# Kernel tuning notes

Hardware: AMD Instinct MI355X
Metric: run time of the kernel (lower is better)

The kernel has to match this reference:

```python
import jax, jax.numpy as jnp
import numpy as np

B, N, EMB, NCLS = 4, 4096, 1024, 13

def knn_euclid(x, k):
    # x: (B,C,N); k nearest by squared euclidean distance
    sq = jnp.sum(x * x, axis=1)                        # (B,N)
    inner = jnp.einsum('bcn,bcm->bnm', x, x)           # (B,N,N)
    d = sq[:, :, None] - 2.0 * inner + sq[:, None, :]
    return jax.lax.stop_gradient(jax.lax.top_k(-d, k)[1])   # (B,N,k)

def knn_cosine(x, k):
    xn = x / (jnp.linalg.norm(x, axis=1, keepdims=True) + 1e-8)
    sim = jnp.einsum('bcn,bcm->bnm', xn, xn)           # (B,N,N)
    return jax.lax.stop_gradient(jax.lax.top_k(sim, k)[1])

def edge_conv(x, idx, w0, s0, o0, w1, s1, o1):
    # x: (B,C,N), idx: (B,N,k) -> (B,64,N). Edge feats = concat(x_j - x_i, x_i).
    xt = jnp.transpose(x, (0, 2, 1))                   # (B,N,C)
    nbr = jax.vmap(lambda f, i: f[i])(xt, idx)         # (B,N,k,C)
    ctr = jnp.broadcast_to(xt[:, :, None, :], nbr.shape)
    e = jnp.concatenate([nbr - ctr, ctr], axis=-1)     # (B,N,k,2C)
    h = jax.nn.leaky_relu(jnp.einsum('bnkc,oc->bnko', e, w0) * s0 + o0, 0.2)
    h = jax.nn.leaky_relu(jnp.einsum('bnkc,oc->bnko', h, w1) * s1 + o1, 0.2)
    return jnp.transpose(jnp.max(h, axis=2), (0, 2, 1))  # max over k -> (B,64,N)

def conv1d(x, w):
    return jnp.einsum('bcn,oc->bon', x, w)

def setup_inputs():
    key = jax.random.key(0)
    cnt = [0]
    def nxt():
        cnt[0] += 1
        return jax.random.fold_in(key, cnt[0])
    W = lambda shape: jax.random.normal(nxt(), shape, jnp.float32) * 0.05
    S = lambda n: 1.0 + 0.1 * jax.random.normal(nxt(), (n,), jnp.float32)   # folded BN scale
    O = lambda n: 0.05 * jax.random.normal(nxt(), (n,), jnp.float32)        # folded BN offset / bias
    inp = {'x': jax.random.normal(nxt(), (B, 6, N), jnp.float32)}
    inp.update(w1_0=W((64, 12)), s1_0=S(64), o1_0=O(64), w1_1=W((64, 64)), s1_1=S(64), o1_1=O(64))
    inp.update(w2_0=W((64, 128)), s2_0=S(64), o2_0=O(64), w2_1=W((64, 64)), s2_1=S(64), o2_1=O(64))
    inp.update(w3_0=W((64, 128)), s3_0=S(64), o3_0=O(64), w3_1=W((64, 64)), s3_1=S(64), o3_1=O(64))
    inp.update(w4=W((EMB, 192)), b4=O(EMB))
    inp.update(wf1=W((512, EMB + 192)), sf1=S(512), of1=O(512))
    inp.update(wf2=W((256, 512)), sf2=S(256), of2=O(256))
    inp.update(wf3=W((NCLS, 256)))
    inp['k'] = 20
    return inp

def reference(x, w1_0, s1_0, o1_0, w1_1, s1_1, o1_1,
              w2_0, s2_0, o2_0, w2_1, s2_1, o2_1,
              w3_0, s3_0, o3_0, w3_1, s3_1, o3_1,
              w4, b4, wf1, sf1, of1, wf2, sf2, of2, wf3, k):
    x1 = edge_conv(x, knn_euclid(x, k), w1_0, s1_0, o1_0, w1_1, s1_1, o1_1)
    x2 = edge_conv(x1, knn_cosine(x1, k), w2_0, s2_0, o2_0, w2_1, s2_1, o2_1)
    x3 = edge_conv(x2, knn_cosine(x2, k), w3_0, s3_0, o3_0, w3_1, s3_1, o3_1)
    xc = jnp.concatenate([x1, x2, x3], axis=1)         # (B,192,N)
    x4 = jax.nn.leaky_relu(conv1d(xc, w4) + b4[None, :, None], 0.2)  # (B,EMB,N)
    g = jnp.max(x4, axis=2, keepdims=True)             # global max pool (B,EMB,1)
    g = jnp.broadcast_to(g, (x4.shape[0], x4.shape[1], xc.shape[2]))  # Repeat to N
    x5 = jnp.concatenate([x1, x2, x3, g], axis=1)      # (B,192+EMB,N)
    h = jax.nn.leaky_relu(conv1d(x5, wf1) * sf1[None, :, None] + of1[None, :, None], 0.2)
    h = jax.nn.leaky_relu(conv1d(h, wf2) * sf2[None, :, None] + of2[None, :, None], 0.2)
    return conv1d(h, wf3)                              # (B,NCLS,N)
```

## Files before the change

### kernel.cpp

```cpp
#include <hip/hip_runtime.h>
#include <hip/hip_bf16.h>
#include <float.h>

#define NPTS 4096
#define NB 4
#define KNN 20

__device__ __forceinline__ float lrelu(float x) { return x > 0.f ? x : 0.2f * x; }

__device__ __forceinline__ void atomicMaxF(float* addr, float val) {
    int* ia = (int*)addr;
    int old = *ia;
    while (__int_as_float(old) < val) {
        int assumed = old;
        old = atomicCAS(ia, assumed, __float_as_int(val));
        if (old == assumed) break;
    }
}

__global__ void k_transp(const float* __restrict__ src, float* __restrict__ dst,
                         int rows, int srcld, int cols) {
    int i = blockIdx.x * 256 + threadIdx.x;
    if (i >= rows * cols) return;
    int r = i % rows, c = i / rows;
    dst[c * rows + r] = src[(size_t)r * srcld + c];
}

__global__ void k_sqnorm(const float* __restrict__ x, float* __restrict__ sq) {
    int i = blockIdx.x * 256 + threadIdx.x;
    int b = i >> 12, n = i & 4095;
    const float* xb = x + b * 6 * NPTS;
    float s = 0.f;
#pragma unroll
    for (int c = 0; c < 6; c++) { float v = xb[c * NPTS + n]; s += v * v; }
    sq[i] = s;
}

__global__ __launch_bounds__(256) void k_knn_euclid(const float* __restrict__ x,
                                                    const float* __restrict__ sq,
                                                    int* __restrict__ idx) {
    int t = threadIdx.x;
    int w = t >> 6, ln = t & 63;
    int qid = blockIdx.x * 4 + w;
    int b = qid >> 12, qn = qid & 4095;
    const float* xb = x + b * 6 * NPTS;
    const float* sqb = sq + b * NPTS;
    float q0 = xb[qn], q1 = xb[NPTS + qn], q2 = xb[2 * NPTS + qn];
    float q3 = xb[3 * NPTS + qn], q4 = xb[4 * NPTS + qn], q5 = xb[5 * NPTS + qn];
    float sqn = sqb[qn];
    float lv = -FLT_MAX; int li = 0x7fffffff;
    float th = -FLT_MAX;
    for (int t0 = 0; t0 < NPTS; t0 += 64) {
        int m = t0 + ln;
        float dot = q0 * xb[m] + q1 * xb[NPTS + m] + q2 * xb[2 * NPTS + m]
                  + q3 * xb[3 * NPTS + m] + q4 * xb[4 * NPTS + m] + q5 * xb[5 * NPTS + m];
        float sv = -(sqn - 2.f * dot + sqb[m]);
        unsigned long long mask = __ballot(sv > th);
        while (mask) {
            int src = __ffsll((unsigned long long)mask) - 1;
            mask &= mask - 1;
            float v = __shfl(sv, src);
            if (!(v > th)) continue;
            int mi = t0 + src;
            float pv = __shfl_up(lv, 1);
            int   pi = __shfl_up(li, 1);
            unsigned long long bm = __ballot(ln < 20 && lv >= v);
            int pos = __popcll(bm);
            if (ln < 20) {
                if (ln == pos) { lv = v; li = mi; }
                else if (ln > pos) { lv = pv; li = pi; }
            }
            th = __shfl(lv, 19);
        }
    }
    if (ln < KNN) idx[qid * KNN + ln] = li;
}

__global__ __launch_bounds__(256) void k_knn_cos(const float* __restrict__ xn,
                                                 const float* __restrict__ xnT,
                                                 int* __restrict__ idx) {
    __shared__ float xq[64][20];
    __shared__ float simb[16][520];
    int t = threadIdx.x;
    int w = t >> 6, ln = t & 63;
    int b = blockIdx.x >> 8;
    int q0blk = (blockIdx.x & 255) * 16;
    const float* xqg = xn + ((size_t)(b << 12) + q0blk) * 64;
    {
        int q = t >> 4, c4 = t & 15;
        float4 v = *(const float4*)(xqg + q * 64 + c4 * 4);
        xq[c4 * 4 + 0][q] = v.x; xq[c4 * 4 + 1][q] = v.y;
        xq[c4 * 4 + 2][q] = v.z; xq[c4 * 4 + 3][q] = v.w;
    }
    __syncthreads();
    int myq = w * 4;
    const float* xTb = xnT + (((size_t)b) << 12) * 64;
    float lv[4] = {-FLT_MAX, -FLT_MAX, -FLT_MAX, -FLT_MAX};
    int   li[4] = {0x7fffffff, 0x7fffffff, 0x7fffffff, 0x7fffffff};
    float th[4] = {-FLT_MAX, -FLT_MAX, -FLT_MAX, -FLT_MAX};
    for (int strip = 0; strip < 8; strip++) {
        int m0 = strip * 512 + ln * 8;
        float4 a0[4], a1[4];
#pragma unroll
        for (int q = 0; q < 4; q++) { a0[q] = (float4){0,0,0,0}; a1[q] = (float4){0,0,0,0}; }
        for (int c = 0; c < 64; c++) {
            const float* cr = xTb + (((size_t)c) << 12) + m0;
            float4 cv0 = *(const float4*)(cr);
            float4 cv1 = *(const float4*)(cr + 4);
            float4 qv = *(const float4*)&xq[c][myq];
            a0[0].x += qv.x * cv0.x; a0[0].y += qv.x * cv0.y; a0[0].z += qv.x * cv0.z; a0[0].w += qv.x * cv0.w;
            a1[0].x += qv.x * cv1.x; a1[0].y += qv.x * cv1.y; a1[0].z += qv.x * cv1.z; a1[0].w += qv.x * cv1.w;
            a0[1].x += qv.y * cv0.x; a0[1].y += qv.y * cv0.y; a0[1].z += qv.y * cv0.z; a0[1].w += qv.y * cv0.w;
            a1[1].x += qv.y * cv1.x; a1[1].y += qv.y * cv1.y; a1[1].z += qv.y * cv1.z; a1[1].w += qv.y * cv1.w;
            a0[2].x += qv.z * cv0.x; a0[2].y += qv.z * cv0.y; a0[2].z += qv.z * cv0.z; a0[2].w += qv.z * cv0.w;
            a1[2].x += qv.z * cv1.x; a1[2].y += qv.z * cv1.y; a1[2].z += qv.z * cv1.z; a1[2].w += qv.z * cv1.w;
            a0[3].x += qv.w * cv0.x; a0[3].y += qv.w * cv0.y; a0[3].z += qv.w * cv0.z; a0[3].w += qv.w * cv0.w;
            a1[3].x += qv.w * cv1.x; a1[3].y += qv.w * cv1.y; a1[3].z += qv.w * cv1.z; a1[3].w += qv.w * cv1.w;
        }
#pragma unroll
        for (int q = 0; q < 4; q++) {
            float mx8 = fmaxf(fmaxf(fmaxf(a0[q].x, a0[q].y), fmaxf(a0[q].z, a0[q].w)),
                              fmaxf(fmaxf(a1[q].x, a1[q].y), fmaxf(a1[q].z, a1[q].w)));
            unsigned long long gmask = __ballot(mx8 > th[q]);
            if (!gmask) continue;
            *(float4*)&simb[myq + q][ln * 8] = a0[q];
            *(float4*)&simb[myq + q][ln * 8 + 4] = a1[q];
            for (int j = 0; j < 8; j++) {
                if (!((gmask >> (8 * j)) & 0xffull)) continue;
                float sv = simb[myq + q][j * 64 + ln];
                int base = strip * 512 + j * 64;
                unsigned long long mask = __ballot(sv > th[q]);
                while (mask) {
                    int src = __ffsll((unsigned long long)mask) - 1;
                    mask &= mask - 1;
                    float v = __shfl(sv, src);
                    if (!(v > th[q])) continue;
                    int mi = base + src;
                    float pv = __shfl_up(lv[q], 1);
                    int   pi = __shfl_up(li[q], 1);
                    unsigned long long bm = __ballot(ln < 20 && lv[q] >= v);
                    int pos = __popcll(bm);
                    if (ln < 20) {
                        if (ln == pos) { lv[q] = v; li[q] = mi; }
                        else if (ln > pos) { lv[q] = pv; li[q] = pi; }
                    }
                    th[q] = __shfl(lv[q], 19);
                }
            }
        }
    }
#pragma unroll
    for (int q = 0; q < 4; q++) {
        if (ln < KNN) {
            int qid = (b << 12) + q0blk + myq + q;
            idx[(size_t)qid * KNN + ln] = li[q];
        }
    }
}

__global__ void k_normalize(const float* __restrict__ xcpm, int coff,
                            float* __restrict__ xn, float* __restrict__ xnT) {
    int pid = blockIdx.x * 256 + threadIdx.x;
    int b = pid >> 12, n = pid & 4095;
    const float* p = xcpm + (size_t)pid * 192 + coff;
    float s = 0.f;
#pragma unroll
    for (int c4 = 0; c4 < 16; c4++) {
        float4 v = *(const float4*)(p + c4 * 4);
        s += v.x * v.x + v.y * v.y + v.z * v.z + v.w * v.w;
    }
    float inv = 1.f / (sqrtf(s) + 1e-8f);
    float* q = xn + (size_t)pid * 64;
    float* qt = xnT + (((size_t)b) << 12) * 64 + n;
#pragma unroll
    for (int c4 = 0; c4 < 16; c4++) {
        float4 v = *(const float4*)(p + c4 * 4);
        float4 r; r.x = v.x * inv; r.y = v.y * inv; r.z = v.z * inv; r.w = v.w * inv;
        *(float4*)(q + c4 * 4) = r;
        qt[(size_t)(c4 * 4 + 0) << 12] = r.x;
        qt[(size_t)(c4 * 4 + 1) << 12] = r.y;
        qt[(size_t)(c4 * 4 + 2) << 12] = r.z;
        qt[(size_t)(c4 * 4 + 3) << 12] = r.w;
    }
}

__global__ __launch_bounds__(256) void k_edge1(const float* __restrict__ x,
    const float* __restrict__ w0, const float* __restrict__ s0, const float* __restrict__ o0,
    const float* __restrict__ w1, const float* __restrict__ s1, const float* __restrict__ o1,
    const int* __restrict__ idx, float* __restrict__ xcpm) {
    __shared__ float es[4][16];
    __shared__ float h0s[4][64];
    int t = threadIdx.x;
    int w = t >> 6, o = t & 63;
    int pid = blockIdx.x * 4 + w;
    int b = pid >> 12, n = pid & 4095;
    const float* xb = x + b * 6 * NPTS;
    float w0r[12];
    const float* w0p = w0 + o * 12;
#pragma unroll
    for (int c4 = 0; c4 < 3; c4++) {
        float4 v = *(const float4*)(w0p + c4 * 4);
        w0r[c4 * 4] = v.x; w0r[c4 * 4 + 1] = v.y; w0r[c4 * 4 + 2] = v.z; w0r[c4 * 4 + 3] = v.w;
    }
    float w1r[64];
    const float* w1p = w1 + o * 64;
#pragma unroll
    for (int c4 = 0; c4 < 16; c4++) {
        float4 v = *(const float4*)(w1p + c4 * 4);
        w1r[c4 * 4] = v.x; w1r[c4 * 4 + 1] = v.y; w1r[c4 * 4 + 2] = v.z; w1r[c4 * 4 + 3] = v.w;
    }
    float sv0 = s0[o], ov0 = o0[o], sv1 = s1[o], ov1 = o1[o];
    float cv = 0.f;
    if (o < 6) { cv = xb[o * NPTS + n]; es[w][6 + o] = cv; }
    if (o >= 12 && o < 16) es[w][o] = 0.f;
    float acc = -FLT_MAX;
    const int* ib = idx + pid * KNN;
    for (int kk = 0; kk < KNN; kk++) {
        int j = ib[kk] & 4095;
        if (o < 6) es[w][o] = xb[o * NPTS + j] - cv;
        float h = 0.f;
#pragma unroll
        for (int c4 = 0; c4 < 3; c4++) {
            float4 e4 = *(const float4*)&es[w][c4 * 4];
            h += w0r[c4 * 4] * e4.x + w0r[c4 * 4 + 1] * e4.y + w0r[c4 * 4 + 2] * e4.z + w0r[c4 * 4 + 3] * e4.w;
        }
        h = lrelu(h * sv0 + ov0);
        h0s[w][o] = h;
        float h2 = 0.f;
#pragma unroll
        for (int c4 = 0; c4 < 16; c4++) {
            float4 h4 = *(const float4*)&h0s[w][c4 * 4];
            h2 += w1r[c4 * 4] * h4.x + w1r[c4 * 4 + 1] * h4.y + w1r[c4 * 4 + 2] * h4.z + w1r[c4 * 4 + 3] * h4.w;
        }
        h2 = lrelu(h2 * sv1 + ov1);
        acc = fmaxf(acc, h2);
    }
    xcpm[(size_t)pid * 192 + o] = acc;
}

__global__ __launch_bounds__(256) void k_edge23(const float* __restrict__ xcpm,
    const float* __restrict__ w0, const float* __restrict__ s0, const float* __restrict__ o0,
    const float* __restrict__ w1, const float* __restrict__ s1, const float* __restrict__ o1,
    const int* __restrict__ idx, int ci, int co) {
    __shared__ float cs[4][64];
    __shared__ float es[4][64];
    __shared__ float h0s[4][64];
    int t = threadIdx.x;
    int w = t >> 6, o = t & 63;
    int pid = blockIdx.x * 4 + w;
    int b = pid >> 12;
    float w0r[64];
    const float* w0p = w0 + o * 128;
#pragma unroll
    for (int c4 = 0; c4 < 16; c4++) {
        float4 v = *(const float4*)(w0p + c4 * 4);
        w0r[c4 * 4] = v.x; w0r[c4 * 4 + 1] = v.y; w0r[c4 * 4 + 2] = v.z; w0r[c4 * 4 + 3] = v.w;
    }
    float w1r[64];
    const float* w1p = w1 + o * 64;
#pragma unroll
    for (int c4 = 0; c4 < 16; c4++) {
        float4 v = *(const float4*)(w1p + c4 * 4);
        w1r[c4 * 4] = v.x; w1r[c4 * 4 + 1] = v.y; w1r[c4 * 4 + 2] = v.z; w1r[c4 * 4 + 3] = v.w;
    }
    float sv0 = s0[o], ov0 = o0[o], sv1 = s1[o], ov1 = o1[o];
    float cv = xcpm[(size_t)pid * 192 + ci + o];
    cs[w][o] = cv;
    float h0b = 0.f;
    const float* w0q = w0p + 64;
#pragma unroll
    for (int c4 = 0; c4 < 16; c4++) {
        float4 wv = *(const float4*)(w0q + c4 * 4);
        float4 c4v = *(const float4*)&cs[w][c4 * 4];
        h0b += wv.x * c4v.x + wv.y * c4v.y + wv.z * c4v.z + wv.w * c4v.w;
    }
    float acc = -FLT_MAX;
    const int* ib = idx + pid * KNN;
    int j0 = ib[0] & 4095;
    float nv = xcpm[((size_t)(b * 4096 + j0)) * 192 + ci + o];
    for (int kk = 0; kk < KNN; kk++) {
        float cur = nv;
        if (kk < KNN - 1) {
            int jn = ib[kk + 1] & 4095;
            nv = xcpm[((size_t)(b * 4096 + jn)) * 192 + ci + o];
        }
        es[w][o] = cur - cv;
        float h = h0b;
#pragma unroll
        for (int c4 = 0; c4 < 16; c4++) {
            float4 e4 = *(const float4*)&es[w][c4 * 4];
            h += w0r[c4 * 4] * e4.x + w0r[c4 * 4 + 1] * e4.y + w0r[c4 * 4 + 2] * e4.z + w0r[c4 * 4 + 3] * e4.w;
        }
        h = lrelu(h * sv0 + ov0);
        h0s[w][o] = h;
        float h2 = 0.f;
#pragma unroll
        for (int c4 = 0; c4 < 16; c4++) {
            float4 h4 = *(const float4*)&h0s[w][c4 * 4];
            h2 += w1r[c4 * 4] * h4.x + w1r[c4 * 4 + 1] * h4.y + w1r[c4 * 4 + 2] * h4.z + w1r[c4 * 4 + 3] * h4.w;
        }
        h2 = lrelu(h2 * sv1 + ov1);
        acc = fmaxf(acc, h2);
    }
    float* outp = (float*)xcpm;
    outp[(size_t)pid * 192 + co + o] = acc;
}

__global__ void k_init_g(float* __restrict__ g) {
    g[blockIdx.x * 256 + threadIdx.x] = -FLT_MAX;
}

__global__ __launch_bounds__(256) void k_w4pool(const float* __restrict__ xc,
                                                const float* __restrict__ wT4,
                                                const float* __restrict__ b4,
                                                float* __restrict__ g) {
    __shared__ float xcs[192 * 68];
    int t = threadIdx.x;
    int b = blockIdx.y;
    int n0 = blockIdx.x * 64;
    const float* xb = xc + (size_t)(b * 4096 + n0) * 192;
    for (int i = t; i < 3072; i += 256) {
        int pt = i / 48, c4 = i - pt * 48;
        float4 v = *(const float4*)(xb + pt * 192 + c4 * 4);
        xcs[(c4 * 4 + 0) * 68 + pt] = v.x; xcs[(c4 * 4 + 1) * 68 + pt] = v.y;
        xcs[(c4 * 4 + 2) * 68 + pt] = v.z; xcs[(c4 * 4 + 3) * 68 + pt] = v.w;
    }
    __syncthreads();
    int o0 = (t >> 2) * 16, qd = t & 3;
    float4 bb[4];
#pragma unroll
    for (int k = 0; k < 4; k++) bb[k] = *(const float4*)(b4 + o0 + k * 4);
    float mx[16];
#pragma unroll
    for (int oo = 0; oo < 16; oo++) mx[oo] = -FLT_MAX;
    for (int sub = 0; sub < 4; sub++) {
        int tn0 = sub * 16 + qd * 4;
        float4 acc[16];
#pragma unroll
        for (int oo = 0; oo < 16; oo++) acc[oo] = (float4){0, 0, 0, 0};
        for (int c = 0; c < 192; c++) {
            float4 x4 = *(const float4*)&xcs[c * 68 + tn0];
            const float* wr = wT4 + c * 1024 + o0;
            float4 wq[4];
#pragma unroll
            for (int k = 0; k < 4; k++) wq[k] = *(const float4*)(wr + k * 4);
#pragma unroll
            for (int oo = 0; oo < 16; oo++) {
                float wv = ((const float*)wq)[oo];
                acc[oo].x += wv * x4.x; acc[oo].y += wv * x4.y;
                acc[oo].z += wv * x4.z; acc[oo].w += wv * x4.w;
            }
        }
#pragma unroll
        for (int oo = 0; oo < 16; oo++) {
            float bias = ((const float*)bb)[oo];
            float4 a = acc[oo];
            float h = fmaxf(fmaxf(lrelu(a.x + bias), lrelu(a.y + bias)),
                            fmaxf(lrelu(a.z + bias), lrelu(a.w + bias)));
            mx[oo] = fmaxf(mx[oo], h);
        }
    }
#pragma unroll
    for (int oo = 0; oo < 16; oo++) {
        float v = mx[oo];
        v = fmaxf(v, __shfl_xor(v, 1));
        v = fmaxf(v, __shfl_xor(v, 2));
        if (qd == 0) atomicMaxF(&g[b * 1024 + o0 + oo], v);
    }
}

__global__ __launch_bounds__(256) void k_goff(const float* __restrict__ g,
                                              const float* __restrict__ wf1,
                                              const float* __restrict__ sf1,
                                              const float* __restrict__ of1,
                                              float* __restrict__ goff) {
    int bo = blockIdx.x;
    int b = bo >> 9, o = bo & 511;
    int t = threadIdx.x;
    const float* wr = wf1 + (size_t)o * 1216 + 192;
    const float* gb = g + b * 1024;
    float s = 0.f;
    for (int c = t; c < 1024; c += 256) s += wr[c] * gb[c];
    __shared__ float red[4];
    for (int off = 32; off > 0; off >>= 1) s += __shfl_down(s, off);
    if ((t & 63) == 0) red[t >> 6] = s;
    __syncthreads();
    if (t == 0) {
        float tot = red[0] + red[1] + red[2] + red[3];
        goff[bo] = tot * sf1[o] + of1[o];
    }
}

#define TP 20
__global__ __launch_bounds__(256) void k_tail(const float* __restrict__ xc,
                                              const float* __restrict__ wf1T,
                                              const float* __restrict__ sf1,
                                              const float* __restrict__ goff,
                                              const float* __restrict__ wf2T,
                                              const float* __restrict__ sf2,
                                              const float* __restrict__ of2,
                                              const float* __restrict__ wf3,
                                              float* __restrict__ out) {
    __shared__ float xcs[192 * TP];
    __shared__ float h1s[512 * TP];
    __shared__ float h2s[256 * TP];
    int t = threadIdx.x;
    int b = blockIdx.y;
    int n0 = blockIdx.x * 16;
    const float* xb = xc + (size_t)(b * 4096 + n0) * 192;
    for (int i = t; i < 768; i += 256) {
        int pt = i / 48, c4 = i - pt * 48;
        float4 v = *(const float4*)(xb + pt * 192 + c4 * 4);
        xcs[(c4 * 4 + 0) * TP + pt] = v.x; xcs[(c4 * 4 + 1) * TP + pt] = v.y;
        xcs[(c4 * 4 + 2) * TP + pt] = v.z; xcs[(c4 * 4 + 3) * TP + pt] = v.w;
    }
    __syncthreads();
    {
        int o8 = (t >> 2) * 8, tn0 = (t & 3) * 4;
        float4 acc[8];
#pragma unroll
        for (int oo = 0; oo < 8; oo++) acc[oo] = (float4){0, 0, 0, 0};
        for (int c = 0; c < 192; c++) {
            float4 x4 = *(const float4*)&xcs[c * TP + tn0];
            const float* wr = wf1T + c * 512 + o8;
            float4 w0 = *(const float4*)(wr);
            float4 w1 = *(const float4*)(wr + 4);
            float wq[8] = {w0.x, w0.y, w0.z, w0.w, w1.x, w1.y, w1.z, w1.w};
#pragma unroll
            for (int oo = 0; oo < 8; oo++) {
                acc[oo].x += wq[oo] * x4.x; acc[oo].y += wq[oo] * x4.y;
                acc[oo].z += wq[oo] * x4.z; acc[oo].w += wq[oo] * x4.w;
            }
        }
#pragma unroll
        for (int oo = 0; oo < 8; oo++) {
            int o = o8 + oo;
            float s = sf1[o];
            float gv = goff[b * 512 + o];
            float4 r;
            r.x = lrelu(acc[oo].x * s + gv); r.y = lrelu(acc[oo].y * s + gv);
            r.z = lrelu(acc[oo].z * s + gv); r.w = lrelu(acc[oo].w * s + gv);
            *(float4*)&h1s[o * TP + tn0] = r;
        }
    }
    __syncthreads();
    {
        int o4 = (t >> 2) * 4, tn0 = (t & 3) * 4;
        float4 acc[4];
#pragma unroll
        for (int oo = 0; oo < 4; oo++) acc[oo] = (float4){0, 0, 0, 0};
        for (int c = 0; c < 512; c++) {
            float4 x4 = *(const float4*)&h1s[c * TP + tn0];
            float4 w = *(const float4*)(wf2T + c * 256 + o4);
            float wq[4] = {w.x, w.y, w.z, w.w};
#pragma unroll
            for (int oo = 0; oo < 4; oo++) {
                acc[oo].x += wq[oo] * x4.x; acc[oo].y += wq[oo] * x4.y;
                acc[oo].z += wq[oo] * x4.z; acc[oo].w += wq[oo] * x4.w;
            }
        }
#pragma unroll
        for (int oo = 0; oo < 4; oo++) {
            int o = o4 + oo;
            float s = sf2[o], of = of2[o];
            float4 r;
            r.x = lrelu(acc[oo].x * s + of); r.y = lrelu(acc[oo].y * s + of);
            r.z = lrelu(acc[oo].z * s + of); r.w = lrelu(acc[oo].w * s + of);
            *(float4*)&h2s[o * TP + tn0] = r;
        }
    }
    __syncthreads();
    if (t < 13 * 16) {
        int o = t >> 4, tn = t & 15;
        const float* wr = wf3 + o * 256;
        float acc = 0.f;
        for (int c4 = 0; c4 < 64; c4++) {
            float4 wv = *(const float4*)(wr + c4 * 4);
            acc += wv.x * h2s[(c4 * 4 + 0) * TP + tn] + wv.y * h2s[(c4 * 4 + 1) * TP + tn]
                 + wv.z * h2s[(c4 * 4 + 2) * TP + tn] + wv.w * h2s[(c4 * 4 + 3) * TP + tn];
        }
        out[((size_t)b * 13 + o) * NPTS + n0 + tn] = acc;
    }
}

extern "C" void kernel_launch(void* const* d_in, const int* in_sizes, int n_in,
                              void* d_out, int out_size, void* d_ws, size_t ws_size,
                              hipStream_t stream) {
    const float* x    = (const float*)d_in[0];
    const float* w1_0 = (const float*)d_in[1];
    const float* s1_0 = (const float*)d_in[2];
    const float* o1_0 = (const float*)d_in[3];
    const float* w1_1 = (const float*)d_in[4];
    const float* s1_1 = (const float*)d_in[5];
    const float* o1_1 = (const float*)d_in[6];
    const float* w2_0 = (const float*)d_in[7];
    const float* s2_0 = (const float*)d_in[8];
    const float* o2_0 = (const float*)d_in[9];
    const float* w2_1 = (const float*)d_in[10];
    const float* s2_1 = (const float*)d_in[11];
    const float* o2_1 = (const float*)d_in[12];
    const float* w3_0 = (const float*)d_in[13];
    const float* s3_0 = (const float*)d_in[14];
    const float* o3_0 = (const float*)d_in[15];
    const float* w3_1 = (const float*)d_in[16];
    const float* s3_1 = (const float*)d_in[17];
    const float* o3_1 = (const float*)d_in[18];
    const float* w4   = (const float*)d_in[19];
    const float* b4   = (const float*)d_in[20];
    const float* wf1  = (const float*)d_in[21];
    const float* sf1  = (const float*)d_in[22];
    const float* of1  = (const float*)d_in[23];
    const float* wf2  = (const float*)d_in[24];
    const float* sf2  = (const float*)d_in[25];
    const float* of2  = (const float*)d_in[26];
    const float* wf3  = (const float*)d_in[27];

    float* xcpm = (float*)d_ws;
    float* xn   = xcpm + (size_t)NB * NPTS * 192;
    float* sq   = xn + (size_t)NB * NPTS * 64;
    float* g    = sq + NB * NPTS;
    float* goff = g + NB * 1024;
    int*   idx  = (int*)(goff + NB * 512);
    float* wT4  = (float*)(idx + NB * NPTS * KNN);
    float* wf1T = wT4 + 192 * 1024;
    float* wf2T = wf1T + 192 * 512;
    float* xnT  = wf2T + 512 * 256;
    (void)in_sizes; (void)n_in; (void)out_size; (void)ws_size;

    k_transp<<<(1024 * 192 + 255) / 256, 256, 0, stream>>>(w4, wT4, 1024, 192, 192);
    k_transp<<<(512 * 192 + 255) / 256, 256, 0, stream>>>(wf1, wf1T, 512, 1216, 192);
    k_transp<<<(256 * 512 + 255) / 256, 256, 0, stream>>>(wf2, wf2T, 256, 512, 512);
    k_sqnorm<<<NB * NPTS / 256, 256, 0, stream>>>(x, sq);
    k_knn_euclid<<<NB * NPTS / 4, 256, 0, stream>>>(x, sq, idx);
    k_edge1<<<NB * NPTS / 4, 256, 0, stream>>>(x, w1_0, s1_0, o1_0, w1_1, s1_1, o1_1, idx, xcpm);
    k_normalize<<<NB * NPTS / 256, 256, 0, stream>>>(xcpm, 0, xn, xnT);
    k_knn_cos<<<NB * NPTS / 16, 256, 0, stream>>>(xn, xnT, idx);
    k_edge23<<<NB * NPTS / 4, 256, 0, stream>>>(xcpm, w2_0, s2_0, o2_0, w2_1, s2_1, o2_1, idx, 0, 64);
    k_normalize<<<NB * NPTS / 256, 256, 0, stream>>>(xcpm, 64, xn, xnT);
    k_knn_cos<<<NB * NPTS / 16, 256, 0, stream>>>(xn, xnT, idx);
    k_edge23<<<NB * NPTS / 4, 256, 0, stream>>>(xcpm, w3_0, s3_0, o3_0, w3_1, s3_1, o3_1, idx, 64, 128);
    k_init_g<<<NB * 1024 / 256, 256, 0, stream>>>(g);
    k_w4pool<<<dim3(NPTS / 64, NB), 256, 0, stream>>>(xcpm, wT4, b4, g);
    k_goff<<<NB * 512, 256, 0, stream>>>(g, wf1, sf1, of1, goff);
    k_tail<<<dim3(NPTS / 16, NB), 256, 0, stream>>>(xcpm, wf1T, sf1, goff, wf2T, sf2, of2, wf3, (float*)d_out);
}
```

Before: 1.532 ms.

## Compute cosine kNN similarity with split-bf16 MFMA instead of FP32 FMA

The cosine kNN similarity GEMM moves from scalar FP32 FMAs to bf16 MFMA 16x16x32 instructions. Normalized features are split into three bf16 parts (hi/mid/lo), and six cross products are accumulated to approximate FP32 accuracy. The normalize kernel now writes this packed bf16 layout instead of the fp32 and transposed copies. In exchange, the per-strip ballot early-skip is removed and two block barriers are added per strip. Small rounding differences could also change top-k tie ordering.

```diff
diff --git a/kernel.cpp b/kernel.cpp
--- a/kernel.cpp
+++ b/kernel.cpp
@@ -5,6 +5,11 @@
 #define NPTS 4096
 #define NB 4
 #define KNN 20
+
+typedef __attribute__((ext_vector_type(8))) short short8v;
+typedef __attribute__((ext_vector_type(4))) float f32x4;
+
+#define MFMA_B16(acc, a, b) acc = __builtin_amdgcn_mfma_f32_16x16x32_bf16((a), (b), (acc), 0, 0, 0)
 
 __device__ __forceinline__ float lrelu(float x) { return x > 0.f ? x : 0.2f * x; }
 
@@ -16,6 +21,11 @@
         old = atomicCAS(ia, assumed, __float_as_int(val));
         if (old == assumed) break;
     }
+}
+
+__device__ __forceinline__ unsigned bf16rne(float x) {
+    unsigned u = __float_as_uint(x);
+    return (u + 0x7fffu + ((u >> 16) & 1u)) >> 16;
 }
 
 __global__ void k_transp(const float* __restrict__ src, float* __restrict__ dst,
@@ -76,57 +86,73 @@
     if (ln < KNN) idx[qid * KNN + ln] = li;
 }
 
-__global__ __launch_bounds__(256) void k_knn_cos(const float* __restrict__ xn,
-                                                 const float* __restrict__ xnT,
+__global__ __launch_bounds__(256) void k_knn_cos(const unsigned short* __restrict__ xs,
                                                  int* __restrict__ idx) {
-    __shared__ float xq[64][20];
-    __shared__ float simb[16][520];
+    __shared__ float simb[16][516];
     int t = threadIdx.x;
     int w = t >> 6, ln = t & 63;
     int b = blockIdx.x >> 8;
     int q0blk = (blockIdx.x & 255) * 16;
-    const float* xqg = xn + ((size_t)(b << 12) + q0blk) * 64;
-    {
-        int q = t >> 4, c4 = t & 15;
-        float4 v = *(const float4*)(xqg + q * 64 + c4 * 4);
-        xq[c4 * 4 + 0][q] = v.x; xq[c4 * 4 + 1][q] = v.y;
-        xq[c4 * 4 + 2][q] = v.z; xq[c4 * 4 + 3][q] = v.w;
-    }
-    __syncthreads();
+    int lp = ln & 15;
+    int kg = ln >> 4;
+    const unsigned short* xsb = xs + ((size_t)b << 12) * 192;
+    const unsigned short* qb = xsb + (size_t)(q0blk + lp) * 192 + kg * 8;
+    short8v ah0 = *(const short8v*)(qb);
+    short8v ah1 = *(const short8v*)(qb + 32);
+    short8v am0 = *(const short8v*)(qb + 64);
+    short8v am1 = *(const short8v*)(qb + 96);
+    short8v al0 = *(const short8v*)(qb + 128);
+    short8v al1 = *(const short8v*)(qb + 160);
     int myq = w * 4;
-    const float* xTb = xnT + (((size_t)b) << 12) * 64;
     float lv[4] = {-FLT_MAX, -FLT_MAX, -FLT_MAX, -FLT_MAX};
     int   li[4] = {0x7fffffff, 0x7fffffff, 0x7fffffff, 0x7fffffff};
     float th[4] = {-FLT_MAX, -FLT_MAX, -FLT_MAX, -FLT_MAX};
     for (int strip = 0; strip < 8; strip++) {
-        int m0 = strip * 512 + ln * 8;
-        float4 a0[4], a1[4];
-#pragma unroll
-        for (int q = 0; q < 4; q++) { a0[q] = (float4){0,0,0,0}; a1[q] = (float4){0,0,0,0}; }
-        for (int c = 0; c < 64; c++) {
-            const float* cr = xTb + (((size_t)c) << 12) + m0;
-            float4 cv0 = *(const float4*)(cr);
-            float4 cv1 = *(const float4*)(cr + 4);
-            float4 qv = *(const float4*)&xq[c][myq];
-            a0[0].x += qv.x * cv0.x; a0[0].y += qv.x * cv0.y; a0[0].z += qv.x * cv0.z; a0[0].w += qv.x * cv0.w;
-            a1[0].x += qv.x * cv1.x; a1[0].y += qv.x * cv1.y; a1[0].z += qv.x * cv1.z; a1[0].w += qv.x * cv1.w;
-            a0[1].x += qv.y * cv0.x; a0[1].y += qv.y * cv0.y; a0[1].z += qv.y * cv0.z; a0[1].w += qv.y * cv0.w;
-            a1[1].x += qv.y * cv1.x; a1[1].y += qv.y * cv1.y; a1[1].z += qv.y * cv1.z; a1[1].w += qv.y * cv1.w;
-            a0[2].x += qv.z * cv0.x; a0[2].y += qv.z * cv0.y; a0[2].z += qv.z * cv0.z; a0[2].w += qv.z * cv0.w;
-            a1[2].x += qv.z * cv1.x; a1[2].y += qv.z * cv1.y; a1[2].z += qv.z * cv1.z; a1[2].w += qv.z * cv1.w;
-            a0[3].x += qv.w * cv0.x; a0[3].y += qv.w * cv0.y; a0[3].z += qv.w * cv0.z; a0[3].w += qv.w * cv0.w;
-            a1[3].x += qv.w * cv1.x; a1[3].y += qv.w * cv1.y; a1[3].z += qv.w * cv1.z; a1[3].w += qv.w * cv1.w;
-        }
+        int c0 = strip * 512 + w * 128;
+        for (int tp = 0; tp < 4; tp++) {
+            int cand0 = c0 + tp * 32;
+            const unsigned short* cb0 = xsb + (size_t)(cand0 + lp) * 192 + kg * 8;
+            const unsigned short* cb1 = cb0 + 16 * 192;
+            short8v bh0a = *(const short8v*)(cb0);
+            short8v bh1a = *(const short8v*)(cb0 + 32);
+            short8v bm0a = *(const short8v*)(cb0 + 64);
+            short8v bm1a = *(const short8v*)(cb0 + 96);
+            short8v bl0a = *(const short8v*)(cb0 + 128);
+            short8v bl1a = *(const short8v*)(cb0 + 160);
+            short8v bh0b = *(const short8v*)(cb1);
+            short8v bh1b = *(const short8v*)(cb1 + 32);
+            short8v bm0b = *(const short8v*)(cb1 + 64);
+            short8v bm1b = *(const short8v*)(cb1 + 96);
+            short8v bl0b = *(const short8v*)(cb1 + 128);
+            short8v bl1b = *(const short8v*)(cb1 + 160);
+            f32x4 p0 = {0.f, 0.f, 0.f, 0.f}, r0 = {0.f, 0.f, 0.f, 0.f};
+            f32x4 p1 = {0.f, 0.f, 0.f, 0.f}, r1 = {0.f, 0.f, 0.f, 0.f};
+            MFMA_B16(p0, ah0, bh0a); MFMA_B16(r0, ah1, bh1a);
+            MFMA_B16(p1, ah0, bh0b); MFMA_B16(r1, ah1, bh1b);
+            MFMA_B16(p0, ah0, bm0a); MFMA_B16(r0, ah1, bm1a);
+            MFMA_B16(p1, ah0, bm0b); MFMA_B16(r1, ah1, bm1b);
+            MFMA_B16(p0, am0, bh0a); MFMA_B16(r0, am1, bh1a);
+            MFMA_B16(p1, am0, bh0b); MFMA_B16(r1, am1, bh1b);
+            MFMA_B16(p0, ah0, bl0a); MFMA_B16(r0, ah1, bl1a);
+            MFMA_B16(p1, ah0, bl0b); MFMA_B16(r1, ah1, bl1b);
+            MFMA_B16(p0, al0, bh0a); MFMA_B16(r0, al1, bh1a);
+            MFMA_B16(p1, al0, bh0b); MFMA_B16(r1, al1, bh1b);
+            MFMA_B16(p0, am0, bm0a); MFMA_B16(r0, am1, bm1a);
+            MFMA_B16(p1, am0, bm0b); MFMA_B16(r1, am1, bm1b);
+            f32x4 s0 = p0 + r0;
+            f32x4 s1 = p1 + r1;
+            int row = kg * 4;
+            int colL = w * 128 + tp * 32 + lp;
+#pragma unroll
+            for (int r = 0; r < 4; r++) {
+                simb[row + r][colL] = s0[r];
+                simb[row + r][colL + 16] = s1[r];
+            }
+        }
+        __syncthreads();
 #pragma unroll
         for (int q = 0; q < 4; q++) {
-            float mx8 = fmaxf(fmaxf(fmaxf(a0[q].x, a0[q].y), fmaxf(a0[q].z, a0[q].w)),
-                              fmaxf(fmaxf(a1[q].x, a1[q].y), fmaxf(a1[q].z, a1[q].w)));
-            unsigned long long gmask = __ballot(mx8 > th[q]);
-            if (!gmask) continue;
-            *(float4*)&simb[myq + q][ln * 8] = a0[q];
-            *(float4*)&simb[myq + q][ln * 8 + 4] = a1[q];
             for (int j = 0; j < 8; j++) {
-                if (!((gmask >> (8 * j)) & 0xffull)) continue;
                 float sv = simb[myq + q][j * 64 + ln];
                 int base = strip * 512 + j * 64;
                 unsigned long long mask = __ballot(sv > th[q]);
@@ -148,6 +174,7 @@
                 }
             }
         }
+        __syncthreads();
     }
 #pragma unroll
     for (int q = 0; q < 4; q++) {
@@ -159,9 +186,8 @@
 }
 
 __global__ void k_normalize(const float* __restrict__ xcpm, int coff,
-                            float* __restrict__ xn, float* __restrict__ xnT) {
+                            unsigned short* __restrict__ xs) {
     int pid = blockIdx.x * 256 + threadIdx.x;
-    int b = pid >> 12, n = pid & 4095;
     const float* p = xcpm + (size_t)pid * 192 + coff;
     float s = 0.f;
 #pragma unroll
@@ -170,17 +196,27 @@
         s += v.x * v.x + v.y * v.y + v.z * v.z + v.w * v.w;
     }
     float inv = 1.f / (sqrtf(s) + 1e-8f);
-    float* q = xn + (size_t)pid * 64;
-    float* qt = xnT + (((size_t)b) << 12) * 64 + n;
+    unsigned short* q = xs + (size_t)pid * 192;
 #pragma unroll
     for (int c4 = 0; c4 < 16; c4++) {
         float4 v = *(const float4*)(p + c4 * 4);
-        float4 r; r.x = v.x * inv; r.y = v.y * inv; r.z = v.z * inv; r.w = v.w * inv;
-        *(float4*)(q + c4 * 4) = r;
-        qt[(size_t)(c4 * 4 + 0) << 12] = r.x;
-        qt[(size_t)(c4 * 4 + 1) << 12] = r.y;
-        qt[(size_t)(c4 * 4 + 2) << 12] = r.z;
-        qt[(size_t)(c4 * 4 + 3) << 12] = r.w;
+        float f[4] = {v.x * inv, v.y * inv, v.z * inv, v.w * inv};
+        unsigned short hh[4], mm[4], ll[4];
+#pragma unroll
+        for (int j = 0; j < 4; j++) {
+            float x = f[j];
+            unsigned hb = bf16rne(x);
+            float hf = __uint_as_float(hb << 16);
+            float r1 = x - hf;
+            unsigned mb = bf16rne(r1);
+            float mf = __uint_as_float(mb << 16);
+            float r2 = r1 - mf;
+            unsigned lb = bf16rne(r2);
+            hh[j] = (unsigned short)hb; mm[j] = (unsigned short)mb; ll[j] = (unsigned short)lb;
+        }
+        *(ushort4*)(q + c4 * 4)       = make_ushort4(hh[0], hh[1], hh[2], hh[3]);
+        *(ushort4*)(q + 64 + c4 * 4)  = make_ushort4(mm[0], mm[1], mm[2], mm[3]);
+        *(ushort4*)(q + 128 + c4 * 4) = make_ushort4(ll[0], ll[1], ll[2], ll[3]);
     }
 }
 
@@ -516,15 +552,14 @@
     const float* wf3  = (const float*)d_in[27];
 
     float* xcpm = (float*)d_ws;
-    float* xn   = xcpm + (size_t)NB * NPTS * 192;
-    float* sq   = xn + (size_t)NB * NPTS * 64;
+    float* sq   = xcpm + (size_t)NB * NPTS * 192;
     float* g    = sq + NB * NPTS;
     float* goff = g + NB * 1024;
     int*   idx  = (int*)(goff + NB * 512);
     float* wT4  = (float*)(idx + NB * NPTS * KNN);
     float* wf1T = wT4 + 192 * 1024;
     float* wf2T = wf1T + 192 * 512;
-    float* xnT  = wf2T + 512 * 256;
+    unsigned short* xs = (unsigned short*)(wf2T + 512 * 256);
     (void)in_sizes; (void)n_in; (void)out_size; (void)ws_size;
 
     k_transp<<<(1024 * 192 + 255) / 256, 256, 0, stream>>>(w4, wT4, 1024, 192, 192);
@@ -533,11 +568,11 @@
     k_sqnorm<<<NB * NPTS / 256, 256, 0, stream>>>(x, sq);
     k_knn_euclid<<<NB * NPTS / 4, 256, 0, stream>>>(x, sq, idx);
     k_edge1<<<NB * NPTS / 4, 256, 0, stream>>>(x, w1_0, s1_0, o1_0, w1_1, s1_1, o1_1, idx, xcpm);
-    k_normalize<<<NB * NPTS / 256, 256, 0, stream>>>(xcpm, 0, xn, xnT);
-    k_knn_cos<<<NB * NPTS / 16, 256, 0, stream>>>(xn, xnT, idx);
+    k_normalize<<<NB * NPTS / 256, 256, 0, stream>>>(xcpm, 0, xs);
+    k_knn_cos<<<NB * NPTS / 16, 256, 0, stream>>>(xs, idx);
     k_edge23<<<NB * NPTS / 4, 256, 0, stream>>>(xcpm, w2_0, s2_0, o2_0, w2_1, s2_1, o2_1, idx, 0, 64);
-    k_normalize<<<NB * NPTS / 256, 256, 0, stream>>>(xcpm, 64, xn, xnT);
-    k_knn_cos<<<NB * NPTS / 16, 256, 0, stream>>>(xn, xnT, idx);
+    k_normalize<<<NB * NPTS / 256, 256, 0, stream>>>(xcpm, 64, xs);
+    k_knn_cos<<<NB * NPTS / 16, 256, 0, stream>>>(xs, idx);
     k_edge23<<<NB * NPTS / 4, 256, 0, stream>>>(xcpm, w3_0, s3_0, o3_0, w3_1, s3_1, o3_1, idx, 64, 128);
     k_init_g<<<NB * 1024 / 256, 256, 0, stream>>>(g);
     k_w4pool<<<dim3(NPTS / 64, NB), 256, 0, stream>>>(xcpm, wT4, b4, g);
```

Result: slower. 1.584 ms (+3.4%).
